# Kernel optimization log

Hardware: AMD Instinct MI355X
Metric: run time of the kernel (lower is better)

The kernel has to match this reference:

```python
import jax, jax.numpy as jnp
import numpy as np

EMBED = 1024
HEADS = 16
HEAD_DIM = EMBED // HEADS
T = 1024
B = 2
TEMP = 1.0
EPS = 1e-20


def setup_inputs() -> dict:
    key = jax.random.key(0)
    ks = jax.random.split(key, 8)
    s = 0.02  # xavier-ish init scale
    return {
        "g": jax.random.normal(ks[0], (T, B, EMBED), dtype=jnp.float32),
        "h": jax.random.normal(ks[1], (T, B, EMBED), dtype=jnp.float32),
        "g_in_w": jax.random.normal(ks[2], (3 * EMBED, EMBED), dtype=jnp.float32) * s,
        "g_in_b": jnp.zeros((3 * EMBED,), dtype=jnp.float32),
        "h_in_w": jax.random.normal(ks[3], (2 * EMBED, EMBED), dtype=jnp.float32) * s,
        "h_in_b": jnp.zeros((2 * EMBED,), dtype=jnp.float32),
        "g_out_w": jax.random.normal(ks[4], (EMBED, EMBED), dtype=jnp.float32) * s,
        "g_out_b": jnp.zeros((EMBED,), dtype=jnp.float32),
        "h_out_w": jax.random.normal(ks[5], (EMBED, EMBED), dtype=jnp.float32) * s,
        "h_out_b": jnp.zeros((EMBED,), dtype=jnp.float32),
    }


def reference(g, h, g_in_w, g_in_b, h_in_w, h_in_b, g_out_w, g_out_b, h_out_w, h_out_b):
    Tt, Bb, E = g.shape
    H, d = HEADS, HEAD_DIM

    # fused qkv projection on g stream, kv on h stream (F.linear: x @ W^T + b)
    q, gk, gv = jnp.split(g @ g_in_w.T + g_in_b, 3, axis=-1)
    hk, hv = jnp.split(h @ h_in_w.T + h_in_b, 2, axis=-1)
    q = q * (d ** -0.5)

    def to_heads(x):  # [T,B,E] -> [B,H,T,d]
        return x.reshape(Tt, Bb, H, d).transpose(1, 2, 0, 3)

    q, gk, gv, hk, hv = map(to_heads, (q, gk, gv, hk, hv))

    # dual-stream attention scores
    g_scores = jnp.einsum("bhtd,bhsd->bhts", q, gk)
    h_scores = jnp.einsum("bhtd,bhsd->bhts", q, hk)

    g_p = jax.nn.softmax(g_scores, axis=-1)
    h_p = jax.nn.softmax(h_scores, axis=-1)

    # gumbel-softmax sample of h_scores (mode='gumbel', temperature=TEMP)
    u = jax.random.uniform(jax.random.key(42), h_scores.shape, dtype=h_scores.dtype)
    noise = -jnp.log(-jnp.log(u + EPS) + EPS)
    sample = jax.nn.softmax((jax.nn.log_softmax(h_scores, axis=-1) + noise) / TEMP, axis=-1)

    g_attn = jnp.einsum("bhts,bhsd->bhtd", g_p, gv)
    h_attn = jnp.einsum("bhts,bhsd->bhtd", sample, hv)

    def merge(x):  # [B,H,T,d] -> [T,B,E]
        return x.transpose(2, 0, 1, 3).reshape(Tt, Bb, E)

    g_out = merge(g_attn) @ g_out_w.T + g_out_b
    h_out = merge(h_attn) @ h_out_w.T + h_out_b
    return g_out, h_out
```

## Files before the change

### kernel.cpp

```cpp
#include <hip/hip_runtime.h>
#include <stdint.h>

#define T_SEQ 1024

typedef __attribute__((ext_vector_type(8))) short short8;
typedef __attribute__((ext_vector_type(4))) float f32x4;
typedef __attribute__((ext_vector_type(4))) unsigned short ushort4v;
typedef __attribute__((ext_vector_type(8))) unsigned short ushort8v;

__device__ __forceinline__ unsigned short f2bf(float f) {
  union { float f; uint32_t u; } v; v.f = f;
  return (unsigned short)((v.u + 0x7fffu + ((v.u >> 16) & 1u)) >> 16);
}
__device__ __forceinline__ float bf2f(unsigned short u) {
  union { uint32_t u; float f; } v; v.u = ((uint32_t)u) << 16;
  return v.f;
}

__device__ __forceinline__ uint32_t tf_bits(uint32_t flat) {
  const uint32_t ks1 = 42u;
  const uint32_t ks2 = 0x1BD11BDAu ^ 42u;
  uint32_t x0 = 0u;
  uint32_t x1 = flat + ks1;
#define TFR(r) { x0 += x1; x1 = (x1 << (r)) | (x1 >> (32 - (r))); x1 ^= x0; }
  TFR(13) TFR(15) TFR(26) TFR(6)
  x0 += ks1; x1 += ks2 + 1u;
  TFR(17) TFR(29) TFR(16) TFR(24)
  x0 += ks2; x1 += 2u;
  TFR(13) TFR(15) TFR(26) TFR(6)
  x1 += ks1 + 3u;
  TFR(17) TFR(29) TFR(16) TFR(24)
  x0 += ks1; x1 += ks2 + 4u;
  TFR(13) TFR(15) TFR(26) TFR(6)
  x0 += ks2; x1 += 5u;
#undef TFR
  return x0 ^ x1;
}

__device__ __forceinline__ float gumbel_noise(uint32_t flat) {
  const uint32_t bits = tf_bits(flat);
  const float u = __uint_as_float((bits >> 9) | 0x3f800000u) - 1.0f;
  return -__logf(-__logf(u + 1e-20f) + 1e-20f);
}

__global__ __launch_bounds__(256) void convert_pre(
    const float* __restrict__ g, const float* __restrict__ h,
    const float* __restrict__ wgi_f, const float* __restrict__ whi_f,
    const float* __restrict__ wgo_f, const float* __restrict__ who_f,
    unsigned short* __restrict__ ghi, unsigned short* __restrict__ glo,
    unsigned short* __restrict__ hhi, unsigned short* __restrict__ hlo,
    unsigned short* __restrict__ wgi, unsigned short* __restrict__ whi,
    unsigned short* __restrict__ wgo, unsigned short* __restrict__ who)
{
  const int64_t Q_SPLIT = 1048576;
  const int64_t Q_TOTAL = Q_SPLIT + 1835008;
  for (int64_t qd = (int64_t)blockIdx.x * 256 + threadIdx.x; qd < Q_TOTAL;
       qd += (int64_t)gridDim.x * 256) {
    if (qd < Q_SPLIT) {
      const int which = qd >= 524288;
      const int64_t e = (qd - (which ? 524288 : 0)) * 4;
      const float4 v = *(const float4*)((which ? h : g) + e);
      ushort4v hi = {f2bf(v.x), f2bf(v.y), f2bf(v.z), f2bf(v.w)};
      ushort4v lo = {f2bf(v.x - bf2f(hi[0])), f2bf(v.y - bf2f(hi[1])),
                     f2bf(v.z - bf2f(hi[2])), f2bf(v.w - bf2f(hi[3]))};
      *(ushort4v*)((which ? hhi : ghi) + e) = hi;
      *(ushort4v*)((which ? hlo : glo) + e) = lo;
    } else {
      int64_t off = qd - Q_SPLIT;
      const float* src; unsigned short* dst;
      if (off < 786432)                 { src = wgi_f; dst = wgi; }
      else if (off < 1310720)           { off -= 786432;  src = whi_f; dst = whi; }
      else if (off < 1572864)           { off -= 1310720; src = wgo_f; dst = wgo; }
      else                              { off -= 1572864; src = who_f; dst = who; }
      const int64_t e = off * 4;
      const float4 v = *(const float4*)(src + e);
      ushort4v u = {f2bf(v.x), f2bf(v.y), f2bf(v.z), f2bf(v.w)};
      *(ushort4v*)(dst + e) = u;
    }
  }
}

template<bool SPLIT, bool BF16OUT>
__device__ __forceinline__ void gemm_bf16_core(
    const unsigned short* __restrict__ Ahi_g, const unsigned short* __restrict__ Alo_g,
    const unsigned short* __restrict__ Wg_, const float* __restrict__ bias,
    int N, int K, int m0, int n0, int scale_limit, void* Cout,
    unsigned short* sA, unsigned short* sL, unsigned short* sW)
{
  const int tid = threadIdx.x;
  const int srow = tid >> 1;
  const int scol = (tid & 1) << 5;
  const int w = tid >> 6;
  const int wr = (w >> 1) << 6, wc = (w & 1) << 6;
  const int lane = tid & 63;
  const int txl = lane & 15, q = lane >> 4;

  f32x4 acc[4][4];
#pragma unroll
  for (int i = 0; i < 4; i++)
#pragma unroll
    for (int j = 0; j < 4; j++) acc[i][j] = (f32x4){0.f, 0.f, 0.f, 0.f};

  for (int k0 = 0; k0 < K; k0 += 64) {
    const unsigned short* Ap = Ahi_g + (size_t)(m0 + srow) * K + k0 + scol;
    const unsigned short* Lp = Alo_g + (size_t)(m0 + srow) * K + k0 + scol;
    const unsigned short* Wp = Wg_  + (size_t)(n0 + srow) * K + k0 + scol;
    ushort8v a8[4], l8[4], w8[4];
#pragma unroll
    for (int e = 0; e < 4; e++) {
      a8[e] = *(const ushort8v*)(Ap + 8 * e);
      if (SPLIT) l8[e] = *(const ushort8v*)(Lp + 8 * e);
      w8[e] = *(const ushort8v*)(Wp + 8 * e);
    }
    __syncthreads();
#pragma unroll
    for (int e = 0; e < 4; e++) {
      *(ushort8v*)&sA[srow * 72 + scol + 8 * e] = a8[e];
      if (SPLIT) *(ushort8v*)&sL[srow * 72 + scol + 8 * e] = l8[e];
      *(ushort8v*)&sW[srow * 72 + scol + 8 * e] = w8[e];
    }
    __syncthreads();
#pragma unroll
    for (int kk = 0; kk < 2; kk++) {
      short8 af[4], al[4], wf[4];
#pragma unroll
      for (int i = 0; i < 4; i++) {
        af[i] = *(const short8*)&sA[(wr + 16 * i + txl) * 72 + 32 * kk + 8 * q];
        if (SPLIT) al[i] = *(const short8*)&sL[(wr + 16 * i + txl) * 72 + 32 * kk + 8 * q];
      }
#pragma unroll
      for (int j = 0; j < 4; j++)
        wf[j] = *(const short8*)&sW[(wc + 16 * j + txl) * 72 + 32 * kk + 8 * q];
#pragma unroll
      for (int i = 0; i < 4; i++)
#pragma unroll
        for (int j = 0; j < 4; j++) {
          acc[i][j] = __builtin_amdgcn_mfma_f32_16x16x32_bf16(af[i], wf[j], acc[i][j], 0, 0, 0);
          if (SPLIT)
            acc[i][j] = __builtin_amdgcn_mfma_f32_16x16x32_bf16(al[i], wf[j], acc[i][j], 0, 0, 0);
        }
    }
  }

#pragma unroll
  for (int j = 0; j < 4; j++) {
    const int col = n0 + wc + 16 * j + txl;
    const float bj = bias[col];
    const float sc = (col < scale_limit) ? 0.125f : 1.0f;
#pragma unroll
    for (int i = 0; i < 4; i++) {
      const int rbase = m0 + wr + 16 * i + 4 * q;
#pragma unroll
      for (int r = 0; r < 4; r++) {
        const float v = (acc[i][j][r] + bj) * sc;
        if (BF16OUT) ((unsigned short*)Cout)[(size_t)(rbase + r) * N + col] = f2bf(v);
        else         ((float*)Cout)[(size_t)(rbase + r) * N + col] = v;
      }
    }
  }
}

__global__ __launch_bounds__(256, 2) void gemm_inproj(
    const unsigned short* __restrict__ ghi, const unsigned short* __restrict__ glo,
    const unsigned short* __restrict__ wgi, const float* __restrict__ bgi,
    const unsigned short* __restrict__ hhi, const unsigned short* __restrict__ hlo,
    const unsigned short* __restrict__ whi, const float* __restrict__ bhi,
    unsigned short* __restrict__ qkv, unsigned short* __restrict__ hkv)
{
  __shared__ __align__(16) unsigned short sm[27648];
  const int bx = blockIdx.x;
  const int m0 = blockIdx.y * 128;
  if (bx < 24)
    gemm_bf16_core<true, true>(ghi, glo, wgi, bgi, 3072, 1024, m0, bx * 128, 1024,
                               qkv, sm, sm + 9216, sm + 18432);
  else
    gemm_bf16_core<true, true>(hhi, hlo, whi, bhi, 2048, 1024, m0, (bx - 24) * 128, 0,
                               hkv, sm, sm + 9216, sm + 18432);
}

__global__ __launch_bounds__(256, 2) void gemm_outproj(
    const unsigned short* __restrict__ attnb,
    const unsigned short* __restrict__ wgo, const float* __restrict__ bgo,
    const unsigned short* __restrict__ who, const float* __restrict__ bho,
    float* __restrict__ out)
{
  __shared__ __align__(16) unsigned short sm[18432];
  const int m0 = blockIdx.y * 128;
  const unsigned short* Wp = (m0 < 2048) ? wgo : who;
  const float* bp = (m0 < 2048) ? bgo : bho;
  gemm_bf16_core<false, false>(attnb, attnb, Wp, bp, 1024, 1024, m0, blockIdx.x * 128, 0,
                               out, sm, sm, sm + 9216);
}

__global__ __launch_bounds__(256, 4) void attn_mfma(
    const unsigned short* __restrict__ qkv, const unsigned short* __restrict__ hkv,
    float* __restrict__ Opart, float* __restrict__ lpart)
{
  __shared__ __align__(16) unsigned short smem[18432];
  unsigned short* KV = smem;
  unsigned short* PC = smem + 9216;
  unsigned short* QS = smem + 9216;

  const int tid = threadIdx.x;
  const int w = tid >> 6;
  const int lane = tid & 63;
  const int txl = lane & 15, q = lane >> 4;
  const int t0 = blockIdx.x * 64;
  const int bh = blockIdx.y;
  const int z = blockIdx.z;
  const int b = bh >> 4;
  const int head = bh & 15;
  const int hoff = head * 64;
  const int sr = tid >> 2;
  const int sc = (tid & 3) << 4;

  {
    const size_t gq = ((size_t)(t0 + sr) * 2 + b) * 3072 + hoff + sc;
    *(ushort8v*)&QS[sr * 72 + sc]     = *(const ushort8v*)&qkv[gq];
    *(ushort8v*)&QS[sr * 72 + sc + 8] = *(const ushort8v*)&qkv[gq + 8];
  }
  __syncthreads();
  const short8 aq0 = *(const short8*)&QS[(16 * w + txl) * 72 + 8 * q];
  const short8 aq1 = *(const short8*)&QS[(16 * w + txl) * 72 + 32 + 8 * q];

  f32x4 Og[4], Oh[4];
  float l_g[4], l_h[4];
#pragma unroll
  for (int i = 0; i < 4; i++) {
    Og[i] = (f32x4){0.f, 0.f, 0.f, 0.f};
    Oh[i] = (f32x4){0.f, 0.f, 0.f, 0.f};
    l_g[i] = 0.f; l_h[i] = 0.f;
  }

  unsigned short* pcg = PC + (w * 2 + 0) * 1152;
  unsigned short* pch = PC + (w * 2 + 1) * 1152;

  const int s_begin = z * (T_SEQ / 2);
  const int s_end = s_begin + (T_SEQ / 2);
  for (int s0 = s_begin; s0 < s_end; s0 += 64) {
    __syncthreads();
    {
      const size_t grow = (size_t)(s0 + sr) * 2 + b;
      const ushort8v kg0 = *(const ushort8v*)&qkv[grow * 3072 + 1024 + hoff + sc];
      const ushort8v kg1 = *(const ushort8v*)&qkv[grow * 3072 + 1024 + hoff + sc + 8];
      const ushort8v kh0 = *(const ushort8v*)&hkv[grow * 2048 + hoff + sc];
      const ushort8v kh1 = *(const ushort8v*)&hkv[grow * 2048 + hoff + sc + 8];
      *(ushort8v*)&KV[sr * 72 + sc]            = kg0;
      *(ushort8v*)&KV[sr * 72 + sc + 8]        = kg1;
      *(ushort8v*)&KV[4608 + sr * 72 + sc]     = kh0;
      *(ushort8v*)&KV[4608 + sr * 72 + sc + 8] = kh1;
    }
    __syncthreads();

    f32x4 Sg[4], Sh[4];
    const f32x4 zz = (f32x4){0.f, 0.f, 0.f, 0.f};
#pragma unroll
    for (int nt = 0; nt < 4; nt++) {
      const int srw = (16 * nt + txl) * 72;
      const short8 bg0 = *(const short8*)&KV[srw + 8 * q];
      const short8 bg1 = *(const short8*)&KV[srw + 32 + 8 * q];
      const short8 bh0 = *(const short8*)&KV[4608 + srw + 8 * q];
      const short8 bh1 = *(const short8*)&KV[4608 + srw + 32 + 8 * q];
      f32x4 ag = __builtin_amdgcn_mfma_f32_16x16x32_bf16(aq0, bg0, zz, 0, 0, 0);
      ag = __builtin_amdgcn_mfma_f32_16x16x32_bf16(aq1, bg1, ag, 0, 0, 0);
      f32x4 ah = __builtin_amdgcn_mfma_f32_16x16x32_bf16(aq0, bh0, zz, 0, 0, 0);
      ah = __builtin_amdgcn_mfma_f32_16x16x32_bf16(aq1, bh1, ah, 0, 0, 0);
      Sg[nt] = ag; Sh[nt] = ah;
    }

#pragma unroll
    for (int nt = 0; nt < 4; nt++)
#pragma unroll
      for (int r = 0; r < 4; r++) {
        const uint32_t trow = (uint32_t)(t0 + 16 * w + 4 * q + r);
        const uint32_t scol_ = (uint32_t)(s0 + 16 * nt + txl);
        Sh[nt][r] += gumbel_noise(((uint32_t)bh << 20) | (trow << 10) | scol_);
      }

#pragma unroll
    for (int nt = 0; nt < 4; nt++) {
      float eg[4], eh[4];
#pragma unroll
      for (int r = 0; r < 4; r++) {
        eg[r] = __expf(Sg[nt][r]); l_g[r] += eg[r];
        eh[r] = __expf(Sh[nt][r]); l_h[r] += eh[r];
      }
      const int sbase = (16 * nt + txl) * 18 + 4 * q;
      *(uint32_t*)&pcg[sbase]     = (uint32_t)f2bf(eg[0]) | ((uint32_t)f2bf(eg[1]) << 16);
      *(uint32_t*)&pcg[sbase + 2] = (uint32_t)f2bf(eg[2]) | ((uint32_t)f2bf(eg[3]) << 16);
      *(uint32_t*)&pch[sbase]     = (uint32_t)f2bf(eh[0]) | ((uint32_t)f2bf(eh[1]) << 16);
      *(uint32_t*)&pch[sbase + 2] = (uint32_t)f2bf(eh[2]) | ((uint32_t)f2bf(eh[3]) << 16);
    }

    __syncthreads();
    {
      const int dd = tid >> 2;
      const int sseg = (tid & 3) * 16;
      ushort8v vg[2], vh[2];
#pragma unroll
      for (int p = 0; p < 2; p++)
#pragma unroll
        for (int m = 0; m < 8; m++) {
          const int s = sseg + 8 * p + m;
          const size_t grow = (size_t)(s0 + s) * 2 + b;
          vg[p][m] = qkv[grow * 3072 + 2048 + hoff + dd];
          vh[p][m] = hkv[grow * 2048 + 1024 + hoff + dd];
        }
#pragma unroll
      for (int p = 0; p < 2; p++) {
        *(ushort8v*)&KV[dd * 72 + sseg + 8 * p]        = vg[p];
        *(ushort8v*)&KV[4608 + dd * 72 + sseg + 8 * p] = vh[p];
      }
    }
    __syncthreads();

#pragma unroll
    for (int c = 0; c < 2; c++) {
      short8 apg, aph;
#pragma unroll
      for (int j = 0; j < 8; j++) {
        apg[j] = (short)pcg[(32 * c + 8 * q + j) * 18 + txl];
        aph[j] = (short)pch[(32 * c + 8 * q + j) * 18 + txl];
      }
#pragma unroll
      for (int nt = 0; nt < 4; nt++) {
        const int drow = (16 * nt + txl) * 72;
        const short8 bvg = *(const short8*)&KV[drow + 32 * c + 8 * q];
        const short8 bvh = *(const short8*)&KV[4608 + drow + 32 * c + 8 * q];
        Og[nt] = __builtin_amdgcn_mfma_f32_16x16x32_bf16(apg, bvg, Og[nt], 0, 0, 0);
        Oh[nt] = __builtin_amdgcn_mfma_f32_16x16x32_bf16(aph, bvh, Oh[nt], 0, 0, 0);
      }
    }
  }

  float* opg = Opart + ((size_t)(z * 2 + 0) * 2048) * 1024;
  float* oph = Opart + ((size_t)(z * 2 + 1) * 2048) * 1024;
  float* lpg = lpart + (size_t)(z * 2 + 0) * 2048 * 16;
  float* lph = lpart + (size_t)(z * 2 + 1) * 2048 * 16;
#pragma unroll
  for (int r = 0; r < 4; r++) {
    float lg = l_g[r], lh = l_h[r];
    lg += __shfl_xor(lg, 1); lg += __shfl_xor(lg, 2);
    lg += __shfl_xor(lg, 4); lg += __shfl_xor(lg, 8);
    lh += __shfl_xor(lh, 1); lh += __shfl_xor(lh, 2);
    lh += __shfl_xor(lh, 4); lh += __shfl_xor(lh, 8);
    const int row = (t0 + 16 * w + 4 * q + r) * 2 + b;
    if (txl == 0) {
      lpg[row * 16 + head] = lg;
      lph[row * 16 + head] = lh;
    }
    const size_t base = (size_t)row * 1024 + hoff;
#pragma unroll
    for (int nt = 0; nt < 4; nt++) {
      opg[base + 16 * nt + txl] = Og[nt][r];
      oph[base + 16 * nt + txl] = Oh[nt][r];
    }
  }
}

__global__ __launch_bounds__(256) void merge_attn(
    const float* __restrict__ Opart, const float* __restrict__ lpart,
    unsigned short* __restrict__ attnb)
{
  const int idx = blockIdx.x * 256 + threadIdx.x;
  const int st = idx >> 19;
  const int i = idx & 0x7FFFF;
  const int row = i >> 8;
  const int colq = i & 255;
  const int head = colq >> 4;
  const float4 o0 = *(const float4*)&Opart[((size_t)(0 + st) * 2048 + row) * 1024 + colq * 4];
  const float4 o1 = *(const float4*)&Opart[((size_t)(2 + st) * 2048 + row) * 1024 + colq * 4];
  const float l0 = lpart[(size_t)(0 + st) * 32768 + row * 16 + head];
  const float l1 = lpart[(size_t)(2 + st) * 32768 + row * 16 + head];
  const float inv = 1.0f / (l0 + l1);
  ushort4v u = {f2bf((o0.x + o1.x) * inv), f2bf((o0.y + o1.y) * inv),
                f2bf((o0.z + o1.z) * inv), f2bf((o0.w + o1.w) * inv)};
  *(ushort4v*)&attnb[((size_t)st * 2048 + row) * 1024 + colq * 4] = u;
}

extern "C" void kernel_launch(void* const* d_in, const int* in_sizes, int n_in,
                              void* d_out, int out_size, void* d_ws, size_t ws_size,
                              hipStream_t stream) {
  const float* g       = (const float*)d_in[0];
  const float* h       = (const float*)d_in[1];
  const float* g_in_w  = (const float*)d_in[2];
  const float* g_in_b  = (const float*)d_in[3];
  const float* h_in_w  = (const float*)d_in[4];
  const float* h_in_b  = (const float*)d_in[5];
  const float* g_out_w = (const float*)d_in[6];
  const float* g_out_b = (const float*)d_in[7];
  const float* h_out_w = (const float*)d_in[8];
  const float* h_out_b = (const float*)d_in[9];
  float* out = (float*)d_out;

  unsigned short* ws = (unsigned short*)d_ws;
  unsigned short* qkv   = ws;
  unsigned short* hkv   = qkv + (size_t)2048*3072;
  unsigned short* attnb = hkv + (size_t)2048*2048;
  unsigned short* wgo   = attnb + (size_t)4096*1024;
  unsigned short* who   = wgo + (size_t)1024*1024;
  unsigned short* scratch = who + (size_t)1024*1024;
  unsigned short* ghi = scratch;
  unsigned short* glo = ghi + (size_t)2048*1024;
  unsigned short* hhi = glo + (size_t)2048*1024;
  unsigned short* hlo = hhi + (size_t)2048*1024;
  unsigned short* wgi = hlo + (size_t)2048*1024;
  unsigned short* whi = wgi + (size_t)3072*1024;
  float* Opart = (float*)scratch;
  float* lpart = Opart + (size_t)4*2048*1024;

  convert_pre<<<1024, 256, 0, stream>>>(g, h, g_in_w, h_in_w, g_out_w, h_out_w,
                                        ghi, glo, hhi, hlo, wgi, whi, wgo, who);
  gemm_inproj<<<dim3(40, 16), 256, 0, stream>>>(
      ghi, glo, wgi, g_in_b, hhi, hlo, whi, h_in_b, qkv, hkv);
  attn_mfma<<<dim3(T_SEQ / 64, 32, 2), 256, 0, stream>>>(qkv, hkv, Opart, lpart);
  merge_attn<<<4096, 256, 0, stream>>>(Opart, lpart, attnb);
  gemm_outproj<<<dim3(8, 32), 256, 0, stream>>>(
      attnb, wgo, g_out_b, who, h_out_b, out);
}
```

Measured before the change: 322.5 us.

## Stage GEMM and attention tiles via direct global-to-LDS loads in MFMA fragment layout

Replaces the register-staged global-to-shared copies in the GEMMs and the attention K/Q loads with global_load_lds, writing 16-byte chunks straight into LDS in a per-lane fragment-ordered layout so each MFMA operand becomes one contiguous 16-byte read. This removes the VGPR round-trip and the padded-row layout. The GEMM core is templated on the M tile, and the output projection switches to 64-row tiles with twice as many blocks to raise parallelism. There is no double buffering, so load latency is still exposed at each barrier.

```diff
diff --git a/kernel.cpp b/kernel.cpp
--- a/kernel.cpp
+++ b/kernel.cpp
@@ -7,6 +7,13 @@
 typedef __attribute__((ext_vector_type(4))) float f32x4;
 typedef __attribute__((ext_vector_type(4))) unsigned short ushort4v;
 typedef __attribute__((ext_vector_type(8))) unsigned short ushort8v;
+
+typedef __attribute__((address_space(1))) const unsigned int gu32;
+typedef __attribute__((address_space(3))) unsigned int su32;
+
+__device__ __forceinline__ void glds16(const unsigned short* g, unsigned short* l) {
+  __builtin_amdgcn_global_load_lds((gu32*)g, (su32*)l, 16, 0, 0);
+}
 
 __device__ __forceinline__ unsigned short f2bf(float f) {
   union { float f; uint32_t u; } v; v.f = f;
@@ -80,59 +87,61 @@
   }
 }
 
-template<bool SPLIT, bool BF16OUT>
-__device__ __forceinline__ void gemm_bf16_core(
-    const unsigned short* __restrict__ Ahi_g, const unsigned short* __restrict__ Alo_g,
-    const unsigned short* __restrict__ Wg_, const float* __restrict__ bias,
+template<int TM, bool SPLIT, bool BF16OUT>
+__device__ __forceinline__ void gemm_core2(
+    const unsigned short* __restrict__ Ahi, const unsigned short* __restrict__ Alo,
+    const unsigned short* __restrict__ Wg, const float* __restrict__ bias,
     int N, int K, int m0, int n0, int scale_limit, void* Cout,
     unsigned short* sA, unsigned short* sL, unsigned short* sW)
 {
   const int tid = threadIdx.x;
-  const int srow = tid >> 1;
-  const int scol = (tid & 1) << 5;
   const int w = tid >> 6;
-  const int wr = (w >> 1) << 6, wc = (w & 1) << 6;
   const int lane = tid & 63;
   const int txl = lane & 15, q = lane >> 4;
-
-  f32x4 acc[4][4];
-#pragma unroll
-  for (int i = 0; i < 4; i++)
+  const int wr = (w >> 1) * (TM * 16);
+  const int wc = (w & 1) << 6;
+  const int NA = TM * 4;
+
+  f32x4 acc[TM][4];
+#pragma unroll
+  for (int i = 0; i < TM; i++)
 #pragma unroll
     for (int j = 0; j < 4; j++) acc[i][j] = (f32x4){0.f, 0.f, 0.f, 0.f};
 
   for (int k0 = 0; k0 < K; k0 += 64) {
-    const unsigned short* Ap = Ahi_g + (size_t)(m0 + srow) * K + k0 + scol;
-    const unsigned short* Lp = Alo_g + (size_t)(m0 + srow) * K + k0 + scol;
-    const unsigned short* Wp = Wg_  + (size_t)(n0 + srow) * K + k0 + scol;
-    ushort8v a8[4], l8[4], w8[4];
-#pragma unroll
-    for (int e = 0; e < 4; e++) {
-      a8[e] = *(const ushort8v*)(Ap + 8 * e);
-      if (SPLIT) l8[e] = *(const ushort8v*)(Lp + 8 * e);
-      w8[e] = *(const ushort8v*)(Wp + 8 * e);
-    }
-    __syncthreads();
-#pragma unroll
-    for (int e = 0; e < 4; e++) {
-      *(ushort8v*)&sA[srow * 72 + scol + 8 * e] = a8[e];
-      if (SPLIT) *(ushort8v*)&sL[srow * 72 + scol + 8 * e] = l8[e];
-      *(ushort8v*)&sW[srow * 72 + scol + 8 * e] = w8[e];
-    }
-    __syncthreads();
+    __syncthreads();
+#pragma unroll
+    for (int t = 0; t < NA / 4; t++) {
+      const int a = w * (NA / 4) + t;
+      const int rb = a >> 1, kk = a & 1;
+      const size_t goff = (size_t)(m0 + rb * 16 + txl) * K + k0 + kk * 32 + 8 * q;
+      glds16(Ahi + goff, sA + a * 512);
+      if (SPLIT) glds16(Alo + goff, sL + a * 512);
+    }
+#pragma unroll
+    for (int t = 0; t < 4; t++) {
+      const int a = w * 4 + t;
+      const int rb = a >> 1, kk = a & 1;
+      glds16(Wg + (size_t)(n0 + rb * 16 + txl) * K + k0 + kk * 32 + 8 * q, sW + a * 512);
+    }
+    __syncthreads();
+
 #pragma unroll
     for (int kk = 0; kk < 2; kk++) {
-      short8 af[4], al[4], wf[4];
-#pragma unroll
-      for (int i = 0; i < 4; i++) {
-        af[i] = *(const short8*)&sA[(wr + 16 * i + txl) * 72 + 32 * kk + 8 * q];
-        if (SPLIT) al[i] = *(const short8*)&sL[(wr + 16 * i + txl) * 72 + 32 * kk + 8 * q];
-      }
-#pragma unroll
-      for (int j = 0; j < 4; j++)
-        wf[j] = *(const short8*)&sW[(wc + 16 * j + txl) * 72 + 32 * kk + 8 * q];
-#pragma unroll
-      for (int i = 0; i < 4; i++)
+      short8 af[TM], al[TM], wf[4];
+#pragma unroll
+      for (int i = 0; i < TM; i++) {
+        const int rb = (w >> 1) * TM + i;
+        af[i] = *(const short8*)&sA[(rb * 2 + kk) * 512 + lane * 8];
+        if (SPLIT) al[i] = *(const short8*)&sL[(rb * 2 + kk) * 512 + lane * 8];
+      }
+#pragma unroll
+      for (int j = 0; j < 4; j++) {
+        const int rb = (w & 1) * 4 + j;
+        wf[j] = *(const short8*)&sW[(rb * 2 + kk) * 512 + lane * 8];
+      }
+#pragma unroll
+      for (int i = 0; i < TM; i++)
 #pragma unroll
         for (int j = 0; j < 4; j++) {
           acc[i][j] = __builtin_amdgcn_mfma_f32_16x16x32_bf16(af[i], wf[j], acc[i][j], 0, 0, 0);
@@ -148,7 +157,7 @@
     const float bj = bias[col];
     const float sc = (col < scale_limit) ? 0.125f : 1.0f;
 #pragma unroll
-    for (int i = 0; i < 4; i++) {
+    for (int i = 0; i < TM; i++) {
       const int rbase = m0 + wr + 16 * i + 4 * q;
 #pragma unroll
       for (int r = 0; r < 4; r++) {
@@ -167,15 +176,15 @@
     const unsigned short* __restrict__ whi, const float* __restrict__ bhi,
     unsigned short* __restrict__ qkv, unsigned short* __restrict__ hkv)
 {
-  __shared__ __align__(16) unsigned short sm[27648];
+  __shared__ __align__(16) unsigned short sm[24576];
   const int bx = blockIdx.x;
   const int m0 = blockIdx.y * 128;
   if (bx < 24)
-    gemm_bf16_core<true, true>(ghi, glo, wgi, bgi, 3072, 1024, m0, bx * 128, 1024,
-                               qkv, sm, sm + 9216, sm + 18432);
+    gemm_core2<4, true, true>(ghi, glo, wgi, bgi, 3072, 1024, m0, bx * 128, 1024,
+                              qkv, sm, sm + 8192, sm + 16384);
   else
-    gemm_bf16_core<true, true>(hhi, hlo, whi, bhi, 2048, 1024, m0, (bx - 24) * 128, 0,
-                               hkv, sm, sm + 9216, sm + 18432);
+    gemm_core2<4, true, true>(hhi, hlo, whi, bhi, 2048, 1024, m0, (bx - 24) * 128, 0,
+                              hkv, sm, sm + 8192, sm + 16384);
 }
 
 __global__ __launch_bounds__(256, 2) void gemm_outproj(
@@ -184,12 +193,12 @@
     const unsigned short* __restrict__ who, const float* __restrict__ bho,
     float* __restrict__ out)
 {
-  __shared__ __align__(16) unsigned short sm[18432];
-  const int m0 = blockIdx.y * 128;
+  __shared__ __align__(16) unsigned short sm[12288];
+  const int m0 = blockIdx.y * 64;
   const unsigned short* Wp = (m0 < 2048) ? wgo : who;
   const float* bp = (m0 < 2048) ? bgo : bho;
-  gemm_bf16_core<false, false>(attnb, attnb, Wp, bp, 1024, 1024, m0, blockIdx.x * 128, 0,
-                               out, sm, sm, sm + 9216);
+  gemm_core2<2, false, false>(attnb, attnb, Wp, bp, 1024, 1024, m0, blockIdx.x * 128, 0,
+                              out, sm, sm, sm + 4096);
 }
 
 __global__ __launch_bounds__(256, 4) void attn_mfma(
@@ -211,17 +220,15 @@
   const int b = bh >> 4;
   const int head = bh & 15;
   const int hoff = head * 64;
-  const int sr = tid >> 2;
-  const int sc = (tid & 3) << 4;
-
-  {
-    const size_t gq = ((size_t)(t0 + sr) * 2 + b) * 3072 + hoff + sc;
-    *(ushort8v*)&QS[sr * 72 + sc]     = *(const ushort8v*)&qkv[gq];
-    *(ushort8v*)&QS[sr * 72 + sc + 8] = *(const ushort8v*)&qkv[gq + 8];
-  }
+
+#pragma unroll
+  for (int kk = 0; kk < 2; kk++)
+    glds16(qkv + ((size_t)(t0 + 16 * w + txl) * 2 + b) * 3072 + hoff + 32 * kk + 8 * q,
+           QS + (w * 2 + kk) * 512);
   __syncthreads();
-  const short8 aq0 = *(const short8*)&QS[(16 * w + txl) * 72 + 8 * q];
-  const short8 aq1 = *(const short8*)&QS[(16 * w + txl) * 72 + 32 + 8 * q];
+  const short8 aq0 = *(const short8*)&QS[(w * 2 + 0) * 512 + lane * 8];
+  const short8 aq1 = *(const short8*)&QS[(w * 2 + 1) * 512 + lane * 8];
+  __syncthreads();
 
   f32x4 Og[4], Oh[4];
   float l_g[4], l_h[4];
@@ -239,16 +246,17 @@
   const int s_end = s_begin + (T_SEQ / 2);
   for (int s0 = s_begin; s0 < s_end; s0 += 64) {
     __syncthreads();
-    {
-      const size_t grow = (size_t)(s0 + sr) * 2 + b;
-      const ushort8v kg0 = *(const ushort8v*)&qkv[grow * 3072 + 1024 + hoff + sc];
-      const ushort8v kg1 = *(const ushort8v*)&qkv[grow * 3072 + 1024 + hoff + sc + 8];
-      const ushort8v kh0 = *(const ushort8v*)&hkv[grow * 2048 + hoff + sc];
-      const ushort8v kh1 = *(const ushort8v*)&hkv[grow * 2048 + hoff + sc + 8];
-      *(ushort8v*)&KV[sr * 72 + sc]            = kg0;
-      *(ushort8v*)&KV[sr * 72 + sc + 8]        = kg1;
-      *(ushort8v*)&KV[4608 + sr * 72 + sc]     = kh0;
-      *(ushort8v*)&KV[4608 + sr * 72 + sc + 8] = kh1;
+#pragma unroll
+    for (int t = 0; t < 4; t++) {
+      const int idx = w * 4 + t;
+      const int tile = idx & 7;
+      const int nt = tile >> 1, kk = tile & 1;
+      const unsigned short* gp;
+      if (idx < 8)
+        gp = qkv + ((size_t)(s0 + 16 * nt + txl) * 2 + b) * 3072 + 1024 + hoff + 32 * kk + 8 * q;
+      else
+        gp = hkv + ((size_t)(s0 + 16 * nt + txl) * 2 + b) * 2048 + hoff + 32 * kk + 8 * q;
+      glds16(gp, KV + idx * 512);
     }
     __syncthreads();
 
@@ -256,11 +264,10 @@
     const f32x4 zz = (f32x4){0.f, 0.f, 0.f, 0.f};
 #pragma unroll
     for (int nt = 0; nt < 4; nt++) {
-      const int srw = (16 * nt + txl) * 72;
-      const short8 bg0 = *(const short8*)&KV[srw + 8 * q];
-      const short8 bg1 = *(const short8*)&KV[srw + 32 + 8 * q];
-      const short8 bh0 = *(const short8*)&KV[4608 + srw + 8 * q];
-      const short8 bh1 = *(const short8*)&KV[4608 + srw + 32 + 8 * q];
+      const short8 bg0 = *(const short8*)&KV[(nt * 2 + 0) * 512 + lane * 8];
+      const short8 bg1 = *(const short8*)&KV[(nt * 2 + 1) * 512 + lane * 8];
+      const short8 bh0 = *(const short8*)&KV[(8 + nt * 2 + 0) * 512 + lane * 8];
+      const short8 bh1 = *(const short8*)&KV[(8 + nt * 2 + 1) * 512 + lane * 8];
       f32x4 ag = __builtin_amdgcn_mfma_f32_16x16x32_bf16(aq0, bg0, zz, 0, 0, 0);
       ag = __builtin_amdgcn_mfma_f32_16x16x32_bf16(aq1, bg1, ag, 0, 0, 0);
       f32x4 ah = __builtin_amdgcn_mfma_f32_16x16x32_bf16(aq0, bh0, zz, 0, 0, 0);
@@ -415,6 +422,6 @@
       ghi, glo, wgi, g_in_b, hhi, hlo, whi, h_in_b, qkv, hkv);
   attn_mfma<<<dim3(T_SEQ / 64, 32, 2), 256, 0, stream>>>(qkv, hkv, Opart, lpart);
   merge_attn<<<4096, 256, 0, stream>>>(Opart, lpart, attnb);
-  gemm_outproj<<<dim3(8, 32), 256, 0, stream>>>(
+  gemm_outproj<<<dim3(8, 64), 256, 0, stream>>>(
       attnb, wgo, g_out_b, who, h_out_b, out);
 }
```

Result: slower. 341.0 us (+5.7%).

## Drop hi/lo split-bf16 input projection and retile output projection GEMM

Applied to the files above, without the earlier changes.

Inputs g and h are now converted to a single bf16 copy instead of a hi/lo pair, so the input projection does half the MFMA work, reads half the activation bytes, and uses less shared memory, which allows higher occupancy (launch bound raised to 4). The output projection is retiled to 64-row M tiles with twice as many blocks to fill more CUs. The cost is lower accuracy in the QKV/KV projections, since the residual low bits are no longer accumulated.

```diff
diff --git a/kernel.cpp b/kernel.cpp
--- a/kernel.cpp
+++ b/kernel.cpp
@@ -47,8 +47,7 @@
     const float* __restrict__ g, const float* __restrict__ h,
     const float* __restrict__ wgi_f, const float* __restrict__ whi_f,
     const float* __restrict__ wgo_f, const float* __restrict__ who_f,
-    unsigned short* __restrict__ ghi, unsigned short* __restrict__ glo,
-    unsigned short* __restrict__ hhi, unsigned short* __restrict__ hlo,
+    unsigned short* __restrict__ gbf, unsigned short* __restrict__ hbf,
     unsigned short* __restrict__ wgi, unsigned short* __restrict__ whi,
     unsigned short* __restrict__ wgo, unsigned short* __restrict__ who)
 {
@@ -60,11 +59,8 @@
       const int which = qd >= 524288;
       const int64_t e = (qd - (which ? 524288 : 0)) * 4;
       const float4 v = *(const float4*)((which ? h : g) + e);
-      ushort4v hi = {f2bf(v.x), f2bf(v.y), f2bf(v.z), f2bf(v.w)};
-      ushort4v lo = {f2bf(v.x - bf2f(hi[0])), f2bf(v.y - bf2f(hi[1])),
-                     f2bf(v.z - bf2f(hi[2])), f2bf(v.w - bf2f(hi[3]))};
-      *(ushort4v*)((which ? hhi : ghi) + e) = hi;
-      *(ushort4v*)((which ? hlo : glo) + e) = lo;
+      ushort4v u = {f2bf(v.x), f2bf(v.y), f2bf(v.z), f2bf(v.w)};
+      *(ushort4v*)((which ? hbf : gbf) + e) = u;
     } else {
       int64_t off = qd - Q_SPLIT;
       const float* src; unsigned short* dst;
@@ -80,65 +76,58 @@
   }
 }
 
-template<bool SPLIT, bool BF16OUT>
-__device__ __forceinline__ void gemm_bf16_core(
-    const unsigned short* __restrict__ Ahi_g, const unsigned short* __restrict__ Alo_g,
-    const unsigned short* __restrict__ Wg_, const float* __restrict__ bias,
-    int N, int K, int m0, int n0, int scale_limit, void* Cout,
-    unsigned short* sA, unsigned short* sL, unsigned short* sW)
+template<int TM, bool BF16OUT>
+__device__ __forceinline__ void gemm_plain_core(
+    const unsigned short* __restrict__ Ab, const unsigned short* __restrict__ Wb,
+    const float* __restrict__ bias, int N, int K, int m0, int n0,
+    int scale_limit, void* Cout, unsigned short* sA, unsigned short* sW)
 {
   const int tid = threadIdx.x;
-  const int srow = tid >> 1;
-  const int scol = (tid & 1) << 5;
   const int w = tid >> 6;
-  const int wr = (w >> 1) << 6, wc = (w & 1) << 6;
   const int lane = tid & 63;
   const int txl = lane & 15, q = lane >> 4;
-
-  f32x4 acc[4][4];
-#pragma unroll
-  for (int i = 0; i < 4; i++)
+  const int wr = (w >> 1) * (TM * 16);
+  const int wc = (w & 1) << 6;
+  const int TPR = 8 / TM;
+  const int arow = tid / TPR;
+  const int acol = (tid % TPR) * (8 * TM);
+  const int wrow = tid >> 1;
+  const int wcol = (tid & 1) << 5;
+
+  f32x4 acc[TM][4];
+#pragma unroll
+  for (int i = 0; i < TM; i++)
 #pragma unroll
     for (int j = 0; j < 4; j++) acc[i][j] = (f32x4){0.f, 0.f, 0.f, 0.f};
 
   for (int k0 = 0; k0 < K; k0 += 64) {
-    const unsigned short* Ap = Ahi_g + (size_t)(m0 + srow) * K + k0 + scol;
-    const unsigned short* Lp = Alo_g + (size_t)(m0 + srow) * K + k0 + scol;
-    const unsigned short* Wp = Wg_  + (size_t)(n0 + srow) * K + k0 + scol;
-    ushort8v a8[4], l8[4], w8[4];
-#pragma unroll
-    for (int e = 0; e < 4; e++) {
-      a8[e] = *(const ushort8v*)(Ap + 8 * e);
-      if (SPLIT) l8[e] = *(const ushort8v*)(Lp + 8 * e);
-      w8[e] = *(const ushort8v*)(Wp + 8 * e);
-    }
-    __syncthreads();
-#pragma unroll
-    for (int e = 0; e < 4; e++) {
-      *(ushort8v*)&sA[srow * 72 + scol + 8 * e] = a8[e];
-      if (SPLIT) *(ushort8v*)&sL[srow * 72 + scol + 8 * e] = l8[e];
-      *(ushort8v*)&sW[srow * 72 + scol + 8 * e] = w8[e];
-    }
+    const unsigned short* Ap = Ab + (size_t)(m0 + arow) * K + k0 + acol;
+    const unsigned short* Wp = Wb + (size_t)(n0 + wrow) * K + k0 + wcol;
+    ushort8v a8[TM], w8[4];
+#pragma unroll
+    for (int e = 0; e < TM; e++) a8[e] = *(const ushort8v*)(Ap + 8 * e);
+#pragma unroll
+    for (int e = 0; e < 4; e++)  w8[e] = *(const ushort8v*)(Wp + 8 * e);
+    __syncthreads();
+#pragma unroll
+    for (int e = 0; e < TM; e++) *(ushort8v*)&sA[arow * 72 + acol + 8 * e] = a8[e];
+#pragma unroll
+    for (int e = 0; e < 4; e++)  *(ushort8v*)&sW[wrow * 72 + wcol + 8 * e] = w8[e];
     __syncthreads();
 #pragma unroll
     for (int kk = 0; kk < 2; kk++) {
-      short8 af[4], al[4], wf[4];
-#pragma unroll
-      for (int i = 0; i < 4; i++) {
+      short8 af[TM], wf[4];
+#pragma unroll
+      for (int i = 0; i < TM; i++)
         af[i] = *(const short8*)&sA[(wr + 16 * i + txl) * 72 + 32 * kk + 8 * q];
-        if (SPLIT) al[i] = *(const short8*)&sL[(wr + 16 * i + txl) * 72 + 32 * kk + 8 * q];
-      }
 #pragma unroll
       for (int j = 0; j < 4; j++)
         wf[j] = *(const short8*)&sW[(wc + 16 * j + txl) * 72 + 32 * kk + 8 * q];
 #pragma unroll
-      for (int i = 0; i < 4; i++)
-#pragma unroll
-        for (int j = 0; j < 4; j++) {
+      for (int i = 0; i < TM; i++)
+#pragma unroll
+        for (int j = 0; j < 4; j++)
           acc[i][j] = __builtin_amdgcn_mfma_f32_16x16x32_bf16(af[i], wf[j], acc[i][j], 0, 0, 0);
-          if (SPLIT)
-            acc[i][j] = __builtin_amdgcn_mfma_f32_16x16x32_bf16(al[i], wf[j], acc[i][j], 0, 0, 0);
-        }
     }
   }
 
@@ -148,7 +137,7 @@
     const float bj = bias[col];
     const float sc = (col < scale_limit) ? 0.125f : 1.0f;
 #pragma unroll
-    for (int i = 0; i < 4; i++) {
+    for (int i = 0; i < TM; i++) {
       const int rbase = m0 + wr + 16 * i + 4 * q;
 #pragma unroll
       for (int r = 0; r < 4; r++) {
@@ -160,22 +149,22 @@
   }
 }
 
-__global__ __launch_bounds__(256, 2) void gemm_inproj(
-    const unsigned short* __restrict__ ghi, const unsigned short* __restrict__ glo,
-    const unsigned short* __restrict__ wgi, const float* __restrict__ bgi,
-    const unsigned short* __restrict__ hhi, const unsigned short* __restrict__ hlo,
-    const unsigned short* __restrict__ whi, const float* __restrict__ bhi,
+__global__ __launch_bounds__(256, 4) void gemm_inproj(
+    const unsigned short* __restrict__ gbf, const unsigned short* __restrict__ wgi,
+    const float* __restrict__ bgi,
+    const unsigned short* __restrict__ hbf, const unsigned short* __restrict__ whi,
+    const float* __restrict__ bhi,
     unsigned short* __restrict__ qkv, unsigned short* __restrict__ hkv)
 {
-  __shared__ __align__(16) unsigned short sm[27648];
+  __shared__ __align__(16) unsigned short sm[18432];
   const int bx = blockIdx.x;
   const int m0 = blockIdx.y * 128;
   if (bx < 24)
-    gemm_bf16_core<true, true>(ghi, glo, wgi, bgi, 3072, 1024, m0, bx * 128, 1024,
-                               qkv, sm, sm + 9216, sm + 18432);
+    gemm_plain_core<4, true>(gbf, wgi, bgi, 3072, 1024, m0, bx * 128, 1024,
+                             qkv, sm, sm + 9216);
   else
-    gemm_bf16_core<true, true>(hhi, hlo, whi, bhi, 2048, 1024, m0, (bx - 24) * 128, 0,
-                               hkv, sm, sm + 9216, sm + 18432);
+    gemm_plain_core<4, true>(hbf, whi, bhi, 2048, 1024, m0, (bx - 24) * 128, 0,
+                             hkv, sm, sm + 9216);
 }
 
 __global__ __launch_bounds__(256, 2) void gemm_outproj(
@@ -184,12 +173,12 @@
     const unsigned short* __restrict__ who, const float* __restrict__ bho,
     float* __restrict__ out)
 {
-  __shared__ __align__(16) unsigned short sm[18432];
-  const int m0 = blockIdx.y * 128;
+  __shared__ __align__(16) unsigned short sm[13824];
+  const int m0 = blockIdx.y * 64;
   const unsigned short* Wp = (m0 < 2048) ? wgo : who;
   const float* bp = (m0 < 2048) ? bgo : bho;
-  gemm_bf16_core<false, false>(attnb, attnb, Wp, bp, 1024, 1024, m0, blockIdx.x * 128, 0,
-                               out, sm, sm, sm + 9216);
+  gemm_plain_core<2, false>(attnb, Wp, bp, 1024, 1024, m0, blockIdx.x * 128, 0,
+                            out, sm, sm + 4608);
 }
 
 __global__ __launch_bounds__(256, 4) void attn_mfma(
@@ -400,21 +389,19 @@
   unsigned short* wgo   = attnb + (size_t)4096*1024;
   unsigned short* who   = wgo + (size_t)1024*1024;
   unsigned short* scratch = who + (size_t)1024*1024;
-  unsigned short* ghi = scratch;
-  unsigned short* glo = ghi + (size_t)2048*1024;
-  unsigned short* hhi = glo + (size_t)2048*1024;
-  unsigned short* hlo = hhi + (size_t)2048*1024;
-  unsigned short* wgi = hlo + (size_t)2048*1024;
+  unsigned short* gbf = scratch;
+  unsigned short* hbf = gbf + (size_t)2048*1024;
+  unsigned short* wgi = hbf + (size_t)2048*1024;
   unsigned short* whi = wgi + (size_t)3072*1024;
   float* Opart = (float*)scratch;
   float* lpart = Opart + (size_t)4*2048*1024;
 
   convert_pre<<<1024, 256, 0, stream>>>(g, h, g_in_w, h_in_w, g_out_w, h_out_w,
-                                        ghi, glo, hhi, hlo, wgi, whi, wgo, who);
+                                        gbf, hbf, wgi, whi, wgo, who);
   gemm_inproj<<<dim3(40, 16), 256, 0, stream>>>(
-      ghi, glo, wgi, g_in_b, hhi, hlo, whi, h_in_b, qkv, hkv);
+      gbf, wgi, g_in_b, hbf, whi, h_in_b, qkv, hkv);
   attn_mfma<<<dim3(T_SEQ / 64, 32, 2), 256, 0, stream>>>(qkv, hkv, Opart, lpart);
   merge_attn<<<4096, 256, 0, stream>>>(Opart, lpart, attnb);
-  gemm_outproj<<<dim3(8, 32), 256, 0, stream>>>(
+  gemm_outproj<<<dim3(8, 64), 256, 0, stream>>>(
       attnb, wgo, g_out_b, who, h_out_b, out);
 }
```

New measurement: 285.4 us. 11.5% less time.
